# Optimization experiments

Measured on AMD Instinct MI355X. Metric: run time of the kernel, lower is better.

Reference implementation:

```python
import jax, jax.numpy as jnp
import numpy as np

B, F0, D = 4096, 39, 16
CROSS_LAYER_SIZE = (128, 128)


def _he_uniform(key, shape):
    fan_in = int(np.prod(shape[:-1]))
    limit = np.sqrt(6.0 / fan_in)
    return jax.random.uniform(key, shape, jnp.float32, -limit, limit)


def setup_inputs() -> dict:
    key = jax.random.key(0)
    k_x, k_f0, k_f1, k_w, k_b = jax.random.split(key, 5)
    x = jax.random.normal(k_x, (B, F0, D), dtype=jnp.float32)
    # field_nums with direct=False: [39, 128//2=64, 64]
    f0 = _he_uniform(k_f0, (F0 * F0, CROSS_LAYER_SIZE[0]))          # (1521, 128)
    f1 = _he_uniform(k_f1, (F0 * (CROSS_LAYER_SIZE[0] // 2), CROSS_LAYER_SIZE[1]))  # (2496, 128)
    out_dim = CROSS_LAYER_SIZE[0] // 2 + CROSS_LAYER_SIZE[1]        # 192
    dense_w = _he_uniform(k_w, (out_dim, 1))
    dense_b = jnp.zeros((1,), dtype=jnp.float32)
    return {"x": x, "f0": f0, "f1": f1, "dense_w": dense_w, "dense_b": dense_b}


def reference(x, f0, f1, dense_w, dense_b):
    # CIN forward (direct=False, use_bias=False, use_residual=False, relu)
    # x: (B, F0, D)
    filters = [f0, f1]
    n_layers = len(CROSS_LAYER_SIZE)
    h = x  # hidden state, (B, Fk, D)
    finals = []
    for idx, L in enumerate(CROSS_LAYER_SIZE):
        Fk = h.shape[1]
        # filter f_ has shape (F0*Fk, L) with i (field of x0) major, j (field of h) minor
        Wr = filters[idx].reshape(F0, Fk, L)
        # fused outer product + conv1d (kernel width 1 == matmul over i,j):
        # z[b, m, d] = sum_{i,j} x[b,i,d] * h[b,j,d] * W[i,j,m]
        z = jnp.einsum('bid,bjd,ijm->bmd', x, h, Wr)  # (B, L, D)
        z = jax.nn.relu(z)
        if idx != n_layers - 1:
            # split along feature-map axis: first half feeds next layer,
            # second half goes to output
            h = z[:, : L // 2, :]
            finals.append(z[:, L // 2:, :])
        else:
            finals.append(z)
    result = jnp.sum(jnp.concatenate(finals, axis=1), axis=-1)  # (B, 192)
    return result @ dense_w + dense_b  # (B, 1)
```

## Files before the change

kernel.cpp:

```cpp
#include <hip/hip_runtime.h>


typedef __attribute__((ext_vector_type(8)))  short bf16x8;
typedef __attribute__((ext_vector_type(16))) float f32x16;

static __device__ __forceinline__ unsigned short f2bf_rne(float f) {
    unsigned int u = __builtin_bit_cast(unsigned int, f);
    u = (u + 0x7FFFu + ((u >> 16) & 1u)) >> 16;
    return (unsigned short)u;
}
static __device__ __forceinline__ unsigned int pk_trunc(float a, float b) {
    unsigned int ua = __builtin_bit_cast(unsigned int, a);
    unsigned int ub = __builtin_bit_cast(unsigned int, b);
    return (ua >> 16) | (ub & 0xffff0000u);
}

__global__ __launch_bounds__(256)
void CIN_repack(const float* __restrict__ f0, const float* __restrict__ f1,
                unsigned int* __restrict__ ws)
{
    const int tid  = blockIdx.x * 256 + threadIdx.x;
    const int n    = tid & 127;
    const int slot = tid >> 7;
    const int tp   = slot & 3;
    const int half = (slot >> 2) & 1;
    const int kh   = (slot >> 3) & 1;
    const int ch   = slot >> 4;
    const int t0   = tp * 2;
    float v0, v1;
    if (ch < 50) {
        const int ig = ch / 5, jg = ch - ig * 5;
        const int i = ig * 4 + kh * 2 + half;
        const int j = jg * 8 + t0;
        const bool iok = (i < 39);
        v0 = (iok && j     < 39) ? f0[(i * 39 + j    ) * 128 + n] : 0.f;
        v1 = (iok && j + 1 < 39) ? f0[(i * 39 + j + 1) * 128 + n] : 0.f;
    } else {
        const int c1 = ch - 50;
        const int jg = c1 / 5, ig = c1 - jg * 5;
        const int j = jg * 4 + kh * 2 + half;
        const int i = ig * 8 + t0;
        v0 = (i     < 39) ? f1[( i      * 64 + j) * 128 + n] : 0.f;
        v1 = (i + 1 < 39) ? f1[((i + 1) * 64 + j) * 128 + n] : 0.f;
    }
    const int lane = half * 32 + (n & 31);
    const int cg   = n >> 5;
    const int dst  = ch * 2048 + kh * 1024 + cg * 256 + lane * 4 + tp;
    ws[dst] = (unsigned int)f2bf_rne(v0) | ((unsigned int)f2bf_rne(v1) << 16);
}

static __device__ __forceinline__ bf16x8 build8(float xi, float4 a, float4 b) {
    union { unsigned int u[4]; bf16x8 v; } r;
    r.u[0] = pk_trunc(xi * a.x, xi * a.y);
    r.u[1] = pk_trunc(xi * a.z, xi * a.w);
    r.u[2] = pk_trunc(xi * b.x, xi * b.y);
    r.u[3] = pk_trunc(xi * b.z, xi * b.w);
    return r.v;
}

__global__ __launch_bounds__(256, 2)
void CIN_main(const float* __restrict__ x,
              const char* __restrict__ wsB,
              const float* __restrict__ dw,
              const float* __restrict__ db,
              float* __restrict__ out)
{
    __shared__ __align__(16) unsigned short Bsh[2][4096];
    __shared__ __align__(16) float xsTd[8][16][44];
    __shared__ __align__(16) float hsT[8][64][17];
    __shared__ float dws[192];
    __shared__ float red[2][2][4];

    const int tid  = threadIdx.x;
    const int w    = tid >> 6;
    const int lane = tid & 63;
    const int g    = w & 1;
    const int hh   = w >> 1;
    const int half = lane >> 5;
    const int d    = lane & 15;
    const int bsel = (lane >> 4) & 1;
    const int g4   = g * 4;

    auto stage = [&](int ch) {
        const char* src = wsB + (size_t)ch * 8192 + w * 2048 + lane * 16;
        unsigned short* dst = &Bsh[ch & 1][w * 1024];
        __builtin_amdgcn_global_load_lds(
            (const __attribute__((address_space(1))) void*)src,
            (__attribute__((address_space(3))) void*)dst, 16, 0, 0);
        __builtin_amdgcn_global_load_lds(
            (const __attribute__((address_space(1))) void*)(src + 1024),
            (__attribute__((address_space(3))) void*)(dst + 512), 16, 0, 0);
    };
    auto loadB = [&](int ch, bf16x8 (&B)[2][2]) {
        const char* base = (const char*)&Bsh[ch & 1][0] + lane * 16;
#pragma unroll
        for (int kh = 0; kh < 2; ++kh)
#pragma unroll
            for (int c = 0; c < 2; ++c)
                B[kh][c] = *(const bf16x8*)(base + kh * 4096 + (hh * 2 + c) * 1024);
    };

    stage(0);

    const float4* xg4 = (const float4*)(x + (size_t)blockIdx.x * 8 * 624);
    for (int e4 = tid; e4 < 1248; e4 += 256) {
        float4 v = xg4[e4];
        int bb = e4 / 156, r = e4 - bb * 156;
        int i = r >> 2, d0 = (r & 3) * 4;
        xsTd[bb][d0 + 0][i] = v.x; xsTd[bb][d0 + 1][i] = v.y;
        xsTd[bb][d0 + 2][i] = v.z; xsTd[bb][d0 + 3][i] = v.w;
    }
    if (tid < 128) { int bb = tid >> 4, dd = tid & 15; xsTd[bb][dd][39] = 0.f; }
    if (tid < 192) dws[tid] = dw[tid];
    __syncthreads();

    float4 xv[2][10];
#pragma unroll
    for (int p = 0; p < 2; ++p) {
        const float* src = &xsTd[g4 + p * 2 + bsel][d][0];
#pragma unroll
        for (int q = 0; q < 10; ++q) xv[p][q] = *(const float4*)(src + q * 4);
    }

    f32x16 acc[2][2];
#pragma unroll
    for (int p = 0; p < 2; ++p)
#pragma unroll
        for (int c = 0; c < 2; ++c)
#pragma unroll
            for (int r = 0; r < 16; ++r) acc[p][c][r] = 0.f;

    for (int ig = 0; ig < 10; ++ig) {
        float xiv[2][2];
#pragma unroll
        for (int p = 0; p < 2; ++p)
#pragma unroll
            for (int kh = 0; kh < 2; ++kh)
                xiv[p][kh] = xsTd[g4 + p * 2 + bsel][d][ig * 4 + kh * 2 + half];
#pragma unroll
        for (int jg = 0; jg < 5; ++jg) {
            const int ch = ig * 5 + jg;
            stage(ch + 1);
            bf16x8 Bf[2][2];
            loadB(ch, Bf);
            bf16x8 A[2][2];
#pragma unroll
            for (int p = 0; p < 2; ++p)
#pragma unroll
                for (int kh = 0; kh < 2; ++kh)
                    A[p][kh] = build8(xiv[p][kh], xv[p][jg * 2], xv[p][jg * 2 + 1]);
#pragma unroll
            for (int p = 0; p < 2; ++p)
#pragma unroll
                for (int c = 0; c < 2; ++c) {
                    acc[p][c] = __builtin_amdgcn_mfma_f32_32x32x16_bf16(A[p][0], Bf[0][c], acc[p][c], 0, 0, 0);
                    acc[p][c] = __builtin_amdgcn_mfma_f32_32x32x16_bf16(A[p][1], Bf[1][c], acc[p][c], 0, 0, 0);
                }
            __syncthreads();
        }
    }

    float cs[4] = {0.f, 0.f, 0.f, 0.f};
    if (hh == 0) {
#pragma unroll
        for (int p = 0; p < 2; ++p)
#pragma unroll
            for (int c = 0; c < 2; ++c)
#pragma unroll
                for (int r = 0; r < 16; ++r) {
                    const int row = (r & 3) + 8 * (r >> 2) + 4 * half;
                    hsT[g4 + p * 2 + (row >> 4)][c * 32 + (lane & 31)][row & 15] =
                        fmaxf(acc[p][c][r], 0.f);
                }
    } else {
#pragma unroll
        for (int p = 0; p < 2; ++p)
#pragma unroll
            for (int c = 0; c < 2; ++c) {
                const float dwv = dws[c * 32 + (lane & 31)];
#pragma unroll
                for (int r = 0; r < 16; ++r) {
                    const int row = (r & 3) + 8 * (r >> 2) + 4 * half;
                    cs[p * 2 + (row >> 4)] += fmaxf(acc[p][c][r], 0.f) * dwv;
                }
            }
    }
#pragma unroll
    for (int p = 0; p < 2; ++p)
#pragma unroll
        for (int c = 0; c < 2; ++c)
#pragma unroll
            for (int r = 0; r < 16; ++r) acc[p][c][r] = 0.f;
    __syncthreads();

    for (int jg = 0; jg < 16; ++jg) {
        float hjv[2][2];
#pragma unroll
        for (int p = 0; p < 2; ++p)
#pragma unroll
            for (int kh = 0; kh < 2; ++kh)
                hjv[p][kh] = hsT[g4 + p * 2 + bsel][jg * 4 + kh * 2 + half][d];
#pragma unroll
        for (int ig2 = 0; ig2 < 5; ++ig2) {
            const int ch = 50 + jg * 5 + ig2;
            if (ch < 129) stage(ch + 1);
            bf16x8 Bf[2][2];
            loadB(ch, Bf);
            bf16x8 A[2][2];
#pragma unroll
            for (int p = 0; p < 2; ++p)
#pragma unroll
                for (int kh = 0; kh < 2; ++kh)
                    A[p][kh] = build8(hjv[p][kh], xv[p][ig2 * 2], xv[p][ig2 * 2 + 1]);
#pragma unroll
            for (int p = 0; p < 2; ++p)
#pragma unroll
                for (int c = 0; c < 2; ++c) {
                    acc[p][c] = __builtin_amdgcn_mfma_f32_32x32x16_bf16(A[p][0], Bf[0][c], acc[p][c], 0, 0, 0);
                    acc[p][c] = __builtin_amdgcn_mfma_f32_32x32x16_bf16(A[p][1], Bf[1][c], acc[p][c], 0, 0, 0);
                }
            __syncthreads();
        }
    }

#pragma unroll
    for (int p = 0; p < 2; ++p)
#pragma unroll
        for (int c = 0; c < 2; ++c) {
            const float dwv = dws[64 + (2 * hh + c) * 32 + (lane & 31)];
#pragma unroll
            for (int r = 0; r < 16; ++r) {
                const int row = (r & 3) + 8 * (r >> 2) + 4 * half;
                cs[p * 2 + (row >> 4)] += fmaxf(acc[p][c][r], 0.f) * dwv;
            }
        }
#pragma unroll
    for (int rr = 0; rr < 4; ++rr)
#pragma unroll
        for (int off = 32; off > 0; off >>= 1)
            cs[rr] += __shfl_xor(cs[rr], off, 64);
    if (lane == 0) {
#pragma unroll
        for (int rr = 0; rr < 4; ++rr) red[g][hh][rr] = cs[rr];
    }
    __syncthreads();
    if (tid < 8) {
        const int g2 = tid >> 2, rr = tid & 3;
        out[blockIdx.x * 8 + g2 * 4 + rr] = red[g2][0][rr] + red[g2][1][rr] + db[0];
    }
}

extern "C" void kernel_launch(void* const* d_in, const int* in_sizes, int n_in,
                              void* d_out, int out_size, void* d_ws, size_t ws_size,
                              hipStream_t stream)
{
    const float* x  = (const float*)d_in[0];
    const float* f0 = (const float*)d_in[1];
    const float* f1 = (const float*)d_in[2];
    const float* dw = (const float*)d_in[3];
    const float* db = (const float*)d_in[4];
    float* out = (float*)d_out;

    CIN_repack<<<dim3(1040), dim3(256), 0, stream>>>(f0, f1, (unsigned int*)d_ws);
    CIN_main<<<dim3(512), dim3(256), 0, stream>>>(x, (const char*)d_ws, dw, db, out);
}
```

Measured before the change: 137.4 us.

## Load weight fragments directly from global into registers, drop LDS staging and barriers

The main kernel no longer stages filter chunks into shared memory through async global-to-LDS copies followed by a barrier per chunk. Each wave now reads its bf16 weight fragments straight from the packed global buffer into registers, double-buffered two chunks ahead, so the per-chunk __syncthreads disappears. The repack kernel is changed to emit 16-byte packed vectors per thread with fewer blocks, matching the new layout. The risk is higher global/L2 traffic and register pressure, since every wave fetches its own copy rather than sharing one LDS copy.

```diff
diff --git a/kernel.cpp b/kernel.cpp
--- a/kernel.cpp
+++ b/kernel.cpp
@@ -17,36 +17,42 @@
 
 __global__ __launch_bounds__(256)
 void CIN_repack(const float* __restrict__ f0, const float* __restrict__ f1,
-                unsigned int* __restrict__ ws)
+                uint4* __restrict__ ws)
 {
     const int tid  = blockIdx.x * 256 + threadIdx.x;
     const int n    = tid & 127;
     const int slot = tid >> 7;
-    const int tp   = slot & 3;
-    const int half = (slot >> 2) & 1;
-    const int kh   = (slot >> 3) & 1;
-    const int ch   = slot >> 4;
-    const int t0   = tp * 2;
-    float v0, v1;
+    const int half = slot & 1;
+    const int kh   = (slot >> 1) & 1;
+    const int ch   = slot >> 2;
+    float v[8];
     if (ch < 50) {
         const int ig = ch / 5, jg = ch - ig * 5;
         const int i = ig * 4 + kh * 2 + half;
-        const int j = jg * 8 + t0;
         const bool iok = (i < 39);
-        v0 = (iok && j     < 39) ? f0[(i * 39 + j    ) * 128 + n] : 0.f;
-        v1 = (iok && j + 1 < 39) ? f0[(i * 39 + j + 1) * 128 + n] : 0.f;
+#pragma unroll
+        for (int t = 0; t < 8; ++t) {
+            const int j = jg * 8 + t;
+            v[t] = (iok && j < 39) ? f0[(i * 39 + j) * 128 + n] : 0.f;
+        }
     } else {
         const int c1 = ch - 50;
         const int jg = c1 / 5, ig = c1 - jg * 5;
         const int j = jg * 4 + kh * 2 + half;
-        const int i = ig * 8 + t0;
-        v0 = (i     < 39) ? f1[( i      * 64 + j) * 128 + n] : 0.f;
-        v1 = (i + 1 < 39) ? f1[((i + 1) * 64 + j) * 128 + n] : 0.f;
-    }
+#pragma unroll
+        for (int t = 0; t < 8; ++t) {
+            const int i = ig * 8 + t;
+            v[t] = (i < 39) ? f1[(i * 64 + j) * 128 + n] : 0.f;
+        }
+    }
+    uint4 pk;
+    pk.x = (unsigned int)f2bf_rne(v[0]) | ((unsigned int)f2bf_rne(v[1]) << 16);
+    pk.y = (unsigned int)f2bf_rne(v[2]) | ((unsigned int)f2bf_rne(v[3]) << 16);
+    pk.z = (unsigned int)f2bf_rne(v[4]) | ((unsigned int)f2bf_rne(v[5]) << 16);
+    pk.w = (unsigned int)f2bf_rne(v[6]) | ((unsigned int)f2bf_rne(v[7]) << 16);
     const int lane = half * 32 + (n & 31);
     const int cg   = n >> 5;
-    const int dst  = ch * 2048 + kh * 1024 + cg * 256 + lane * 4 + tp;
-    ws[dst] = (unsigned int)f2bf_rne(v0) | ((unsigned int)f2bf_rne(v1) << 16);
+    ws[ch * 512 + kh * 256 + cg * 64 + lane] = pk;
 }
 
 static __device__ __forceinline__ bf16x8 build8(float xi, float4 a, float4 b) {
@@ -65,7 +71,6 @@
               const float* __restrict__ db,
               float* __restrict__ out)
 {
-    __shared__ __align__(16) unsigned short Bsh[2][4096];
     __shared__ __align__(16) float xsTd[8][16][44];
     __shared__ __align__(16) float hsT[8][64][17];
     __shared__ float dws[192];
@@ -81,26 +86,18 @@
     const int bsel = (lane >> 4) & 1;
     const int g4   = g * 4;
 
-    auto stage = [&](int ch) {
-        const char* src = wsB + (size_t)ch * 8192 + w * 2048 + lane * 16;
-        unsigned short* dst = &Bsh[ch & 1][w * 1024];
-        __builtin_amdgcn_global_load_lds(
-            (const __attribute__((address_space(1))) void*)src,
-            (__attribute__((address_space(3))) void*)dst, 16, 0, 0);
-        __builtin_amdgcn_global_load_lds(
-            (const __attribute__((address_space(1))) void*)(src + 1024),
-            (__attribute__((address_space(3))) void*)(dst + 512), 16, 0, 0);
+    const char* wbase = wsB + lane * 16 + hh * 2048 + 2560;
+    bf16x8 Bb[2][2][2];
+    auto loadBg = [&](int ch, bf16x8 (&B)[2][2]) {
+        const char* p0 = wbase + (size_t)ch * 8192;
+        B[0][0] = *(const bf16x8*)(p0 - 2560);
+        B[0][1] = *(const bf16x8*)(p0 - 1536);
+        B[1][0] = *(const bf16x8*)(p0 + 1536);
+        B[1][1] = *(const bf16x8*)(p0 + 2560);
     };
-    auto loadB = [&](int ch, bf16x8 (&B)[2][2]) {
-        const char* base = (const char*)&Bsh[ch & 1][0] + lane * 16;
-#pragma unroll
-        for (int kh = 0; kh < 2; ++kh)
-#pragma unroll
-            for (int c = 0; c < 2; ++c)
-                B[kh][c] = *(const bf16x8*)(base + kh * 4096 + (hh * 2 + c) * 1024);
-    };
-
-    stage(0);
+
+    loadBg(0, Bb[0]);
+    loadBg(1, Bb[1]);
 
     const float4* xg4 = (const float4*)(x + (size_t)blockIdx.x * 8 * 624);
     for (int e4 = tid; e4 < 1248; e4 += 256) {
@@ -130,19 +127,22 @@
 #pragma unroll
             for (int r = 0; r < 16; ++r) acc[p][c][r] = 0.f;
 
-    for (int ig = 0; ig < 10; ++ig) {
-        float xiv[2][2];
-#pragma unroll
-        for (int p = 0; p < 2; ++p)
-#pragma unroll
-            for (int kh = 0; kh < 2; ++kh)
-                xiv[p][kh] = xsTd[g4 + p * 2 + bsel][d][ig * 4 + kh * 2 + half];
-#pragma unroll
-        for (int jg = 0; jg < 5; ++jg) {
-            const int ch = ig * 5 + jg;
-            stage(ch + 1);
-            bf16x8 Bf[2][2];
-            loadB(ch, Bf);
+    float xiv[2][2];
+
+#pragma unroll 1
+    for (int o = 0; o < 5; ++o) {
+#pragma unroll
+        for (int u = 0; u < 10; ++u) {
+            const int ch = o * 10 + u;
+            const int jg = u % 5;
+            if (jg == 0) {
+                const int ib = (o * 2 + u / 5) * 4;
+#pragma unroll
+                for (int p = 0; p < 2; ++p)
+#pragma unroll
+                    for (int kh = 0; kh < 2; ++kh)
+                        xiv[p][kh] = xsTd[g4 + p * 2 + bsel][d][ib + kh * 2 + half];
+            }
             bf16x8 A[2][2];
 #pragma unroll
             for (int p = 0; p < 2; ++p)
@@ -153,10 +153,10 @@
             for (int p = 0; p < 2; ++p)
 #pragma unroll
                 for (int c = 0; c < 2; ++c) {
-                    acc[p][c] = __builtin_amdgcn_mfma_f32_32x32x16_bf16(A[p][0], Bf[0][c], acc[p][c], 0, 0, 0);
-                    acc[p][c] = __builtin_amdgcn_mfma_f32_32x32x16_bf16(A[p][1], Bf[1][c], acc[p][c], 0, 0, 0);
-                }
-            __syncthreads();
+                    acc[p][c] = __builtin_amdgcn_mfma_f32_32x32x16_bf16(A[p][0], Bb[u & 1][0][c], acc[p][c], 0, 0, 0);
+                    acc[p][c] = __builtin_amdgcn_mfma_f32_32x32x16_bf16(A[p][1], Bb[u & 1][1][c], acc[p][c], 0, 0, 0);
+                }
+            loadBg(ch + 2, Bb[u & 1]);
         }
     }
 
@@ -193,33 +193,35 @@
             for (int r = 0; r < 16; ++r) acc[p][c][r] = 0.f;
     __syncthreads();
 
-    for (int jg = 0; jg < 16; ++jg) {
-        float hjv[2][2];
-#pragma unroll
-        for (int p = 0; p < 2; ++p)
-#pragma unroll
-            for (int kh = 0; kh < 2; ++kh)
-                hjv[p][kh] = hsT[g4 + p * 2 + bsel][jg * 4 + kh * 2 + half][d];
-#pragma unroll
-        for (int ig2 = 0; ig2 < 5; ++ig2) {
-            const int ch = 50 + jg * 5 + ig2;
-            if (ch < 129) stage(ch + 1);
-            bf16x8 Bf[2][2];
-            loadB(ch, Bf);
+#pragma unroll 1
+    for (int o2 = 0; o2 < 8; ++o2) {
+#pragma unroll
+        for (int u = 0; u < 10; ++u) {
+            const int ch = 50 + o2 * 10 + u;
+            const int ig2 = u % 5;
+            if (ig2 == 0) {
+                const int jb = (o2 * 2 + u / 5) * 4;
+#pragma unroll
+                for (int p = 0; p < 2; ++p)
+#pragma unroll
+                    for (int kh = 0; kh < 2; ++kh)
+                        xiv[p][kh] = hsT[g4 + p * 2 + bsel][jb + kh * 2 + half][d];
+            }
             bf16x8 A[2][2];
 #pragma unroll
             for (int p = 0; p < 2; ++p)
 #pragma unroll
                 for (int kh = 0; kh < 2; ++kh)
-                    A[p][kh] = build8(hjv[p][kh], xv[p][ig2 * 2], xv[p][ig2 * 2 + 1]);
+                    A[p][kh] = build8(xiv[p][kh], xv[p][ig2 * 2], xv[p][ig2 * 2 + 1]);
 #pragma unroll
             for (int p = 0; p < 2; ++p)
 #pragma unroll
                 for (int c = 0; c < 2; ++c) {
-                    acc[p][c] = __builtin_amdgcn_mfma_f32_32x32x16_bf16(A[p][0], Bf[0][c], acc[p][c], 0, 0, 0);
-                    acc[p][c] = __builtin_amdgcn_mfma_f32_32x32x16_bf16(A[p][1], Bf[1][c], acc[p][c], 0, 0, 0);
-                }
-            __syncthreads();
+                    acc[p][c] = __builtin_amdgcn_mfma_f32_32x32x16_bf16(A[p][0], Bb[u & 1][0][c], acc[p][c], 0, 0, 0);
+                    acc[p][c] = __builtin_amdgcn_mfma_f32_32x32x16_bf16(A[p][1], Bb[u & 1][1][c], acc[p][c], 0, 0, 0);
+                }
+            int chn = ch + 2; if (chn > 129) chn = 129;
+            loadBg(chn, Bb[u & 1]);
         }
     }
 
@@ -261,6 +263,6 @@
     const float* db = (const float*)d_in[4];
     float* out = (float*)d_out;
 
-    CIN_repack<<<dim3(1040), dim3(256), 0, stream>>>(f0, f1, (unsigned int*)d_ws);
+    CIN_repack<<<dim3(260), dim3(256), 0, stream>>>(f0, f1, (uint4*)d_ws);
     CIN_main<<<dim3(512), dim3(256), 0, stream>>>(x, (const char*)d_ws, dw, db, out);
 }
```

Result: faster. 130.6 us (-4.9%).
